# Kernel tuning notes

Hardware: AMD Instinct MI355X
Metric: run time of the kernel (lower is better)

The kernel has to match this reference:

```python
import jax, jax.numpy as jnp
import numpy as np
import math

L = 32            # one_side_length; seq_len = L*L = 1024
EMBED = 768
NDIM = 16
N_SSM = 768
DIRS = 4
K = DIRS * N_SSM  # kernel_dim = 3072
REPEAT = EMBED // N_SSM
SCALE = math.sqrt(1.0 / NDIM)


def _compute_kernel(A_angle, A_radius, B1p, B2p, C1p, C2p):
    # Polar-parameterized complex diagonal A's (4 transition coeffs), sigmoid B, raw C.
    ang = jax.nn.sigmoid(A_angle) * (2.0 * math.pi)
    rad = jax.nn.sigmoid(A_radius)
    A = (rad * jnp.cos(ang) + 1j * (rad * jnp.sin(ang))).astype(jnp.complex64)  # (4,K,NDIM)
    A1, A2, A3, A4 = A[0], A[1], A[2], A[3]
    sB1 = jax.nn.sigmoid(B1p); sB2 = jax.nn.sigmoid(B2p)
    B1 = (sB1[..., 0] + 1j * sB1[..., 1]).astype(jnp.complex64)   # (K,NDIM)
    B2 = (sB2[..., 0] + 1j * sB2[..., 1]).astype(jnp.complex64)
    C1 = (C1p[..., 0] + 1j * C1p[..., 1]).astype(jnp.complex64)
    C2 = (C2p[..., 0] + 1j * C2p[..., 1]).astype(jnp.complex64)

    zeros = jnp.zeros((L, K, NDIM), jnp.complex64)

    # 2-D SSM impulse response (same math the torch module precomputes via the
    # vandermonde / coefficient-table expansion):
    #   x_h[i,j] = A1 x_h[i,j-1] + A2 x_v[i,j-1] + B1 delta[i,j]
    #   x_v[i,j] = A3 x_h[i-1,j] + A4 x_v[i-1,j] + B2 delta[i,j]
    #   k[i,j]   = scale * Re(C1 . x_h[i,j] + C2 . x_v[i,j])
    def row_step(carry, i):
        xh_prev, xv_prev = carry                    # row i-1 states, (L,K,NDIM)
        first = (i == 0).astype(jnp.float32)
        xv = A3 * xh_prev + A4 * xv_prev            # vertical flow from row above
        xv = xv.at[0].add(first * B2)               # impulse at (0,0)
        h0 = (first * B1).astype(jnp.complex64)     # x_h[i,0]
        def col_step(h, v_left):
            h_new = A1 * h + A2 * v_left            # horizontal flow within the row
            return h_new, h_new
        _, xh_rest = jax.lax.scan(col_step, h0, xv[:-1])
        xh = jnp.concatenate([h0[None], xh_rest], axis=0)
        return (xh, xv), (xh, xv)

    (_, _), (XH, XV) = jax.lax.scan(row_step, (zeros, zeros), jnp.arange(L))
    # XH, XV: (L, L, K, NDIM) complex
    k = SCALE * (jnp.einsum('ijhn,hn->ijh', XH, C1) + jnp.einsum('ijhn,hn->ijh', XV, C2))
    # boundary corrections exactly as in the torch module
    k = k.at[0, :, :].multiply(2.0)
    k = k.at[:, 0, :].multiply(2.0)
    k = k.at[0, 0, :].divide(4.0)
    return k.real                                   # (L, L, K) float32


def _forward(x, A_angle, A_radius, B1p, B2p, C1p, C2p, omega):
    S, B, D = x.shape
    residual = x * omega
    k = _compute_kernel(A_angle, A_radius, B1p, B2p, C1p, C2p)
    k = jnp.transpose(k, (2, 0, 1))                 # (K, L, L)
    x4 = jnp.transpose(x, (1, 2, 0)).reshape(B, D, L, L)
    s2 = (2 * L, 2 * L)
    flips = [(), (-2,), (-1,), (-2, -1)]
    out = jnp.zeros((B, D, L, L), jnp.float32)
    for idx, fl in enumerate(flips):                # 4 scan directions via flips
        kk = jnp.tile(k[idx * N_SSM:(idx + 1) * N_SSM], (REPEAT, 1, 1))  # (D,L,L)
        xc = jnp.flip(x4, axis=fl) if fl else x4
        kf = jnp.fft.rfft2(kk, s=s2)
        xf = jnp.fft.rfft2(xc, s=s2)
        cur = jnp.fft.irfft2(xf * kf, s=s2)[..., :L, :L]
        out = out + (jnp.flip(cur, axis=fl) if fl else cur)
    out = jnp.transpose(out.reshape(B, D, S), (2, 0, 1))  # back to (S,B,D)
    return jax.nn.silu(out + residual)


def setup_inputs() -> dict:
    key = jax.random.key(0)
    ks = jax.random.split(key, 9)
    x = jax.random.normal(ks[0], (L * L, 16, EMBED), jnp.float32)
    A_angle = jax.random.uniform(ks[1], (4, K, NDIM), jnp.float32, 0.5, 3.0)
    A_radius = jax.random.uniform(ks[2], (4, K, NDIM), jnp.float32, 0.5, 3.0)
    B1p = 0.2 * jax.random.normal(ks[3], (K, NDIM, 2), jnp.float32)
    B2p = 0.2 * jax.random.normal(ks[4], (K, NDIM, 2), jnp.float32)
    C1p = jax.random.normal(ks[5], (K, NDIM, 2), jnp.float32)
    C2p = jax.random.normal(ks[6], (K, NDIM, 2), jnp.float32)
    omega = jax.random.normal(ks[7], (EMBED,), jnp.float32)
    return {"x": x, "A_angle": A_angle, "A_radius": A_radius, "B1p": B1p,
            "B2p": B2p, "C1p": C1p, "C2p": C2p, "omega": omega}


def reference(x, A_angle, A_radius, B1p, B2p, C1p, C2p, omega):
    return _forward(x, A_angle, A_radius, B1p, B2p, C1p, C2p, omega)
```

## Files before the change

### kernel.cpp

```cpp
#include <hip/hip_runtime.h>
#include <cmath>

#define TWO_PI 6.283185307179586476925f

typedef float f2 __attribute__((ext_vector_type(2)));

__device__ __forceinline__ float sigm(float v) { return 1.0f / (1.0f + __expf(-v)); }
__device__ __forceinline__ f2 mnegi(f2 v) { return (f2){v.y, -v.x}; }
__device__ __forceinline__ f2 mposi(f2 v) { return (f2){-v.y, v.x}; }
__device__ __forceinline__ f2 cmulf(f2 a, f2 b) {
    return (f2){a.x, a.x} * b + (f2){a.y, a.y} * mposi(b);
}
__device__ __forceinline__ f2 cms(f2 A, f2 v) {
    return (f2){A.x, A.x} * v + (f2){A.y, A.y} * (f2){-v.y, v.x};
}

template<int CTRL>
__device__ __forceinline__ float dpp0(float v) {
    return __int_as_float(__builtin_amdgcn_update_dpp(
        0, __float_as_int(v), CTRL, 0xf, 0xf, true));
}
template<int CTRL>
__device__ __forceinline__ f2 dpp2(f2 v) {
    return (f2){dpp0<CTRL>(v.x), dpp0<CTRL>(v.y)};
}
#define DPP_SHR1 0x111
#define DPP_SHR2 0x112
#define DPP_SHR4 0x114
#define DPP_ROR8 0x128

__device__ __forceinline__ float swz_xor16(float v) {
    return __int_as_float(__builtin_amdgcn_ds_swizzle(__float_as_int(v), 0x401F));
}

__device__ __forceinline__ int swz(int r, int c) {
    return (r << 6) | (c ^ ((r ^ (r << 3)) & 63));
}

__device__ __forceinline__ int gfidx(int o, int m, int c) {
    return o + (c << 3) + (m << 9);
}

template<bool INV, bool HALF, bool PRUNE>
__device__ __forceinline__ void dft8(f2* x) {
    const float RS = 0.70710678118654752440f;
    f2 t0, t1, t2, t3, t4, t5, t6, t7;
    if (HALF) {
        t0 = x[0]; t4 = x[0]; t1 = x[1]; t5 = x[1];
        t2 = x[2]; t6 = x[2]; t3 = x[3]; t7 = x[3];
    } else {
        t0 = x[0] + x[4]; t4 = x[0] - x[4];
        t1 = x[1] + x[5]; t5 = x[1] - x[5];
        t2 = x[2] + x[6]; t6 = x[2] - x[6];
        t3 = x[3] + x[7]; t7 = x[3] - x[7];
    }
    f2 t5w, t6w, t7w;
    if (!INV) {
        t5w = RS * (t5 + mnegi(t5));
        t6w = mnegi(t6);
        t7w = RS * (mnegi(t7) - t7);
    } else {
        t5w = RS * (t5 - mnegi(t5));
        t6w = mposi(t6);
        t7w = RS * (mposi(t7) - t7);
    }
    f2 u0 = t0 + t2, u2 = t0 - t2, u1 = t1 + t3, dd = t1 - t3;
    f2 u3 = INV ? mposi(dd) : mnegi(dd);
    x[0] = u0 + u1; x[2] = u2 + u3;
    if (!PRUNE) { x[4] = u0 - u1; x[6] = u2 - u3; }
    f2 v0 = t4 + t6w, v2 = t4 - t6w, v1 = t5w + t7w, ee = t5w - t7w;
    f2 v3 = INV ? mposi(ee) : mnegi(ee);
    x[1] = v0 + v1; x[3] = v2 + v3;
    if (!PRUNE) { x[5] = v0 - v1; x[7] = v2 - v3; }
}

__device__ __forceinline__ void make_tw(int o, f2* tw) {
    float s, co;
    __sincosf(-TWO_PI * (float)o / 64.f, &s, &co);
    tw[0] = (f2){co, s};
#pragma unroll
    for (int k = 1; k < 7; ++k) tw[k] = cmulf(tw[k - 1], tw[0]);
}

template<bool INV, bool COL, bool HALF, bool PRUNE>
__device__ __forceinline__ void fft64(f2* a, f2* r, const f2* tw,
                                      int o, int line) {
    dft8<INV, HALF, false>(r);
#pragma unroll
    for (int k = 1; k < 8; ++k) {
        f2 w = tw[k - 1];
        if (INV) w.y = -w.y;
        r[k] = cmulf(r[k], w);
    }
#pragma unroll
    for (int m = 0; m < 8; ++m) {
        int s = 8 * o + m;
        a[COL ? swz(s, line) : swz(line, s)] = r[m];
    }
#pragma unroll
    for (int j = 0; j < 8; ++j) {
        int s = 8 * j + o;
        r[j] = a[COL ? swz(s, line) : swz(line, s)];
    }
    dft8<INV, false, PRUNE>(r);
}

__global__ __launch_bounds__(512) void ssm_tin(
        const float* __restrict__ Aang, const float* __restrict__ Arad,
        const float* __restrict__ B1p, const float* __restrict__ B2p,
        const float* __restrict__ C1p, const float* __restrict__ C2p,
        f2* __restrict__ Gf, const float* __restrict__ x,
        float* __restrict__ xT) {
    __shared__ __align__(16) char smem[35840];
    int tid = threadIdx.x;

    if (blockIdx.x >= 768) {
        float (*tt)[65] = (float (*)[65])smem;
        int bb = blockIdx.x - 768;
        int bR = bb % 192, bS = bb / 192;
        int r0 = bR * 64, s0 = bS * 64;
        int c = tid & 63, w = tid >> 6;
#pragma unroll
        for (int k = 0; k < 8; ++k) {
            int row = w + 8 * k;
            tt[row][c] = x[(size_t)(s0 + row) * 12288 + r0 + c];
        }
        __syncthreads();
#pragma unroll
        for (int k = 0; k < 8; ++k) {
            int row = w + 8 * k;
            xT[(size_t)(r0 + row) * 1024 + s0 + c] = tt[c][row];
        }
        return;
    }

    f2* a = (f2*)smem;
    float* row0 = (float*)(smem + 32768);
    float* col0 = (float*)(smem + 34816);
    int d = blockIdx.x;
    int w = tid >> 6;
    int t = w & 3;
    int nh = w >> 2;
    int lane = tid & 63;
    int jg = lane & 7;
    int n8 = lane >> 3;
    int n = n8 + 8 * nh;
    int ch = t * 768 + d;
    int gid = ch * 16 + n;

    for (int e = tid; e < 4096; e += 512) a[e] = (f2){0.f, 0.f};
    row0[tid] = 0.f;
    if (tid < 256) col0[tid] = 0.f;

    f2 A[4];
#pragma unroll
    for (int q = 0; q < 4; ++q) {
        float ang = sigm(Aang[q * 49152 + gid]) * TWO_PI;
        float rad = sigm(Arad[q * 49152 + gid]);
        float s, co;
        __sincosf(ang, &s, &co);
        A[q] = (f2){rad * co, rad * s};
    }
    f2 A1 = A[0], A2 = A[1], A3 = A[2], A4 = A[3];
    f2 P2 = cms(A1, A1);
    f2 P3 = cms(A1, P2);
    f2 P4 = cms(P2, P2);
    f2 P8 = cms(P4, P4);
    f2 P16 = cms(P8, P8);
    f2 CZ1 = (jg >= 1) ? P4 : (f2){0.f, 0.f};
    f2 CZ2 = (jg >= 2) ? P8 : (f2){0.f, 0.f};
    f2 CZ4 = (jg >= 4) ? P16 : (f2){0.f, 0.f};

    const float2* B1v = (const float2*)B1p;
    const float2* B2v = (const float2*)B2p;
    const float2* C1v = (const float2*)C1p;
    const float2* C2v = (const float2*)C2p;
    float2 b1 = B1v[gid], b2 = B2v[gid], c1 = C1v[gid], c2 = C2v[gid];
    f2 B1 = (f2){sigm(b1.x), sigm(b1.y)};
    f2 B2 = (f2){sigm(b2.x), sigm(b2.y)};
    float c1r = c1.x, c1i = c1.y, c2r = c2.x, c2i = c2.y;

    f2 pw = (f2){1.f, 0.f};
    if (jg & 1) pw = P4;
    if (jg & 2) pw = cms(pw, P8);
    if (jg & 4) pw = cms(pw, P16);
    f2 EB = cms(pw, B1);

    int bb0 = n8 & 1, bb1 = (n8 >> 1) & 1;
    int col = 4 * jg + 2 * bb0 + bb1;
    int ccl = (t & 2) ? ((64 - col) & 63) : col;

    __syncthreads();

    f2 xv[4], xh[4];
#pragma unroll
    for (int m = 0; m < 4; ++m) { xv[m] = (f2){0.f, 0.f}; xh[m] = (f2){0.f, 0.f}; }

    auto body = [&](int i, bool is0) {
#pragma unroll
        for (int m = 0; m < 4; ++m) xv[m] = cms(A3, xh[m]) + cms(A4, xv[m]);
        if (is0 && jg == 0) xv[0] += B2;
        f2 g1 = cms(A2, xv[0]);
        f2 g2 = cms(A1, g1) + cms(A2, xv[1]);
        f2 g3 = cms(A1, g2) + cms(A2, xv[2]);
        f2 V  = cms(A1, g3) + cms(A2, xv[3]);
        V += cms(CZ1, dpp2<DPP_SHR1>(V));
        V += cms(CZ2, dpp2<DPP_SHR2>(V));
        V += cms(CZ4, dpp2<DPP_SHR4>(V));
        f2 E = dpp2<DPP_SHR1>(V);
        if (jg == 0) E = (f2){0.f, 0.f};
        if (is0) E += EB;
        xh[0] = E;
        xh[1] = cms(A1, E) + g1;
        xh[2] = cms(P2, E) + g2;
        xh[3] = cms(P3, E) + g3;
        float v0 = c1r * xh[0].x - c1i * xh[0].y + c2r * xv[0].x - c2i * xv[0].y;
        float v1 = c1r * xh[1].x - c1i * xh[1].y + c2r * xv[1].x - c2i * xv[1].y;
        float v2 = c1r * xh[2].x - c1i * xh[2].y + c2r * xv[2].x - c2i * xv[2].y;
        float v3 = c1r * xh[3].x - c1i * xh[3].y + c2r * xv[3].x - c2i * xv[3].y;
        float s0 = bb0 ? v0 : v2, s1 = bb0 ? v1 : v3;
        float r0 = dpp0<DPP_ROR8>(s0), r1 = dpp0<DPP_ROR8>(s1);
        float q0 = (bb0 ? v2 : v0) + r0;
        float q1 = (bb0 ? v3 : v1) + r1;
        float s2 = bb1 ? q0 : q1;
        float r2 = swz_xor16(s2);
        float qq = (bb1 ? q1 : q0) + r2;
        qq += __shfl_xor(qq, 32, 64);
        if (n8 < 4) {
            if (is0) {
                row0[(((t << 1) | nh) << 6) | ccl] = qq;
            } else if (col == 0) {
                col0[((((t >> 1) << 1) | nh) << 6) | ((t & 1) ? (64 - i) : i)] = qq;
            } else {
                int rr_ = (t & 1) ? (64 - i) : i;
                ((float*)&a[swz(rr_, ccl)])[nh] = qq;
            }
        }
    };
    body(0, true);
#pragma unroll 1
    for (int i = 1; i < 32; ++i) body(i, false);

    __syncthreads();
    for (int e = tid; e < 4096; e += 512) {
        int r = e >> 6, cm = e & 63;
        int c = cm ^ ((r ^ (r << 3)) & 63);
        f2 cv = a[e];
        float v = cv.x + cv.y;
        if (r == 0) {
            v += row0[c] + row0[64 + c] + row0[128 + c] + row0[192 + c]
               + row0[256 + c] + row0[320 + c] + row0[384 + c] + row0[448 + c];
        } else if (c == 0) {
            v += col0[r] + col0[64 + r] + col0[128 + r] + col0[192 + r];
        }
        float f = 0.25f;
        if (r == 0) f *= 2.f;
        if (c == 0) f *= 2.f;
        if (r == 0 && c == 0) f *= 0.25f;
        a[e] = (f2){f * v, 0.f};
    }
    __syncthreads();
    int o = tid & 7;
    f2 tw[7];
    make_tw(o, tw);
    {
        int row = tid >> 3;
        f2 r[8];
#pragma unroll
        for (int j = 0; j < 8; ++j) r[j] = a[swz(row, 8 * j + o)];
        fft64<false, false, false, false>(a, r, tw, o, row);
#pragma unroll
        for (int m = 0; m < 8; ++m) a[swz(row, o + 8 * m)] = r[m];
    }
    __syncthreads();
    {
        int cc = tid >> 3;
        f2 r[8];
#pragma unroll
        for (int j = 0; j < 8; ++j) r[j] = a[swz(8 * j + o, cc)];
        fft64<false, true, false, false>(a, r, tw, o, cc);
#pragma unroll
        for (int m = 0; m < 8; ++m) Gf[d * 4096 + gfidx(o, m, cc)] = r[m];
    }
}

__global__ __launch_bounds__(512) void conv_fft(
        const float* __restrict__ x, float* __restrict__ xT,
        const f2* __restrict__ Gf, const float* __restrict__ omega,
        float* __restrict__ out, int useT) {
    __shared__ f2 a[8192];
    int bid = (blockIdx.x & 7) * 384 + (blockIdx.x >> 3);
    int d = bid >> 2, b0 = (bid & 3) * 4;
    int tid = threadIdx.x;
    int o = tid & 7, grp = tid >> 3;
    int tl = grp >> 5, row = grp & 31;
    f2 tw[7];
    make_tw(o, tw);
    f2* at = a + (tl << 12);
    int btl = b0 + 2 * tl;
    const size_t base0 = (size_t)(btl * 768 + d) * 1024;
    const size_t base1 = (size_t)((btl + 1) * 768 + d) * 1024;
    {
        f2 r[8];
#pragma unroll
        for (int j = 0; j < 4; ++j) {
            int s2 = row * 32 + 8 * j + o;
            if (useT) r[j] = (f2){xT[base0 + s2], xT[base1 + s2]};
            else      r[j] = (f2){x[s2 * 12288 + btl * 768 + d],
                                  x[s2 * 12288 + (btl + 1) * 768 + d]};
        }
#pragma unroll
        for (int j = 4; j < 8; ++j) r[j] = (f2){0.f, 0.f};
        fft64<false, false, true, false>(at, r, tw, o, row);
#pragma unroll
        for (int m = 0; m < 8; ++m) at[swz(row, o + 8 * m)] = r[m];
    }
    __syncthreads();
#pragma unroll 1
    for (int sw = 0; sw < 2; ++sw) {
        f2* ac = a + (sw << 12);
        int c = grp;
        f2 r[8];
#pragma unroll
        for (int j = 0; j < 4; ++j) r[j] = ac[swz(8 * j + o, c)];
#pragma unroll
        for (int j = 4; j < 8; ++j) r[j] = (f2){0.f, 0.f};
        fft64<false, true, true, false>(ac, r, tw, o, c);
#pragma unroll
        for (int m = 0; m < 8; ++m) {
            r[m] = cmulf(r[m], Gf[d * 4096 + gfidx(o, m, c)]);
        }
        fft64<true, true, false, true>(ac, r, tw, o, c);
#pragma unroll
        for (int m = 0; m < 4; ++m) ac[swz(o + 8 * m, c)] = r[m];
    }
    __syncthreads();
    {
        f2 r[8];
#pragma unroll
        for (int j = 0; j < 8; ++j) r[j] = at[swz(row, 8 * j + o)];
        fft64<true, false, false, true>(at, r, tw, o, row);
        float w = omega[d];
        const float inv = 1.0f / 4096.0f;
#pragma unroll
        for (int m = 0; m < 4; ++m) {
            int cc = o + 8 * m;
            int s2 = row * 32 + cc;
            float xa, xb;
            if (useT) { xa = xT[base0 + s2]; xb = xT[base1 + s2]; }
            else {
                xa = x[s2 * 12288 + btl * 768 + d];
                xb = x[s2 * 12288 + (btl + 1) * 768 + d];
            }
            float ya = r[m].x * inv + xa * w;
            float yb = r[m].y * inv + xb * w;
            float oa = ya / (1.0f + __expf(-ya));
            float ob = yb / (1.0f + __expf(-yb));
            if (useT) {
                xT[base0 + s2] = oa;
                xT[base1 + s2] = ob;
            } else {
                out[s2 * 12288 + btl * 768 + d] = oa;
                out[s2 * 12288 + (btl + 1) * 768 + d] = ob;
            }
        }
    }
}

__global__ __launch_bounds__(256) void transpose_out(const float* __restrict__ xT,
                                                     float* __restrict__ out) {
    __shared__ float t[64][65];
    int bR = blockIdx.x % 192, bS = blockIdx.x / 192;
    int r0 = bR * 64, s0 = bS * 64;
    int c = threadIdx.x & 63, w = threadIdx.x >> 6;
#pragma unroll
    for (int k = 0; k < 16; ++k) {
        int row = w + 4 * k;
        t[row][c] = xT[(size_t)(r0 + row) * 1024 + s0 + c];
    }
    __syncthreads();
#pragma unroll
    for (int k = 0; k < 16; ++k) {
        int row = w + 4 * k;
        out[(size_t)(s0 + row) * 12288 + r0 + c] = t[c][row];
    }
}

extern "C" void kernel_launch(void* const* d_in, const int* in_sizes, int n_in,
                              void* d_out, int out_size, void* d_ws, size_t ws_size,
                              hipStream_t stream) {
    const float* x     = (const float*)d_in[0];
    const float* Aang  = (const float*)d_in[1];
    const float* Arad  = (const float*)d_in[2];
    const float* B1p   = (const float*)d_in[3];
    const float* B2p   = (const float*)d_in[4];
    const float* C1p   = (const float*)d_in[5];
    const float* C2p   = (const float*)d_in[6];
    const float* omega = (const float*)d_in[7];
    float* out = (float*)d_out;
    char* ws = (char*)d_ws;

    f2*    Gf = (f2*)ws;
    float* xT = (float*)(ws + 25165824);
    int useT = (ws_size >= (size_t)75497472) ? 1 : 0;

    int grid1 = useT ? 3840 : 768;
    ssm_tin<<<grid1, 512, 0, stream>>>(Aang, Arad, B1p, B2p, C1p, C2p, Gf, x, xT);
    conv_fft<<<3072, 512, 0, stream>>>(x, xT, Gf, omega, out, useT);
    if (useT) transpose_out<<<3072, 256, 0, stream>>>(xT, out);
}
```

Before: 170.9 us.

## Split conv_fft blocks to one batch pair each and keep inputs in registers

Each conv_fft block now handles a single pair of batches with half the shared memory, and the grid doubles to compensate. The column pass runs once across all 64 thread groups instead of looping twice, while the row passes use only half the threads. The residual input is kept in registers from the first load, so x is not read from global memory a second time. The trade-off is half-idle threads during the row phases and less work per block, in exchange for lower LDS use per block and possibly higher occupancy.

```diff
diff --git a/kernel.cpp b/kernel.cpp
--- a/kernel.cpp
+++ b/kernel.cpp
@@ -288,70 +288,64 @@
         const float* __restrict__ x, float* __restrict__ xT,
         const f2* __restrict__ Gf, const float* __restrict__ omega,
         float* __restrict__ out, int useT) {
-    __shared__ f2 a[8192];
-    int bid = (blockIdx.x & 7) * 384 + (blockIdx.x >> 3);
-    int d = bid >> 2, b0 = (bid & 3) * 4;
+    __shared__ f2 a[4096];
+    int bid = (blockIdx.x & 7) * 768 + (blockIdx.x >> 3);
+    int d = bid >> 3, b = (bid & 7) * 2;
     int tid = threadIdx.x;
     int o = tid & 7, grp = tid >> 3;
-    int tl = grp >> 5, row = grp & 31;
     f2 tw[7];
     make_tw(o, tw);
-    f2* at = a + (tl << 12);
-    int btl = b0 + 2 * tl;
-    const size_t base0 = (size_t)(btl * 768 + d) * 1024;
-    const size_t base1 = (size_t)((btl + 1) * 768 + d) * 1024;
-    {
+    const size_t base0 = (size_t)(b * 768 + d) * 1024;
+    const size_t base1 = (size_t)((b + 1) * 768 + d) * 1024;
+    f2 xsave[4];
+    if (grp < 32) {
+        int row = grp;
         f2 r[8];
 #pragma unroll
         for (int j = 0; j < 4; ++j) {
             int s2 = row * 32 + 8 * j + o;
             if (useT) r[j] = (f2){xT[base0 + s2], xT[base1 + s2]};
-            else      r[j] = (f2){x[s2 * 12288 + btl * 768 + d],
-                                  x[s2 * 12288 + (btl + 1) * 768 + d]};
+            else      r[j] = (f2){x[s2 * 12288 + b * 768 + d],
+                                  x[s2 * 12288 + (b + 1) * 768 + d]};
+            xsave[j] = r[j];
         }
 #pragma unroll
         for (int j = 4; j < 8; ++j) r[j] = (f2){0.f, 0.f};
-        fft64<false, false, true, false>(at, r, tw, o, row);
-#pragma unroll
-        for (int m = 0; m < 8; ++m) at[swz(row, o + 8 * m)] = r[m];
-    }
-    __syncthreads();
-#pragma unroll 1
-    for (int sw = 0; sw < 2; ++sw) {
-        f2* ac = a + (sw << 12);
+        fft64<false, false, true, false>(a, r, tw, o, row);
+#pragma unroll
+        for (int m = 0; m < 8; ++m) a[swz(row, o + 8 * m)] = r[m];
+    }
+    __syncthreads();
+    {
         int c = grp;
         f2 r[8];
 #pragma unroll
-        for (int j = 0; j < 4; ++j) r[j] = ac[swz(8 * j + o, c)];
+        for (int j = 0; j < 4; ++j) r[j] = a[swz(8 * j + o, c)];
 #pragma unroll
         for (int j = 4; j < 8; ++j) r[j] = (f2){0.f, 0.f};
-        fft64<false, true, true, false>(ac, r, tw, o, c);
+        fft64<false, true, true, false>(a, r, tw, o, c);
 #pragma unroll
         for (int m = 0; m < 8; ++m) {
             r[m] = cmulf(r[m], Gf[d * 4096 + gfidx(o, m, c)]);
         }
-        fft64<true, true, false, true>(ac, r, tw, o, c);
-#pragma unroll
-        for (int m = 0; m < 4; ++m) ac[swz(o + 8 * m, c)] = r[m];
-    }
-    __syncthreads();
-    {
+        fft64<true, true, false, true>(a, r, tw, o, c);
+#pragma unroll
+        for (int m = 0; m < 4; ++m) a[swz(o + 8 * m, c)] = r[m];
+    }
+    __syncthreads();
+    if (grp < 32) {
+        int row = grp;
         f2 r[8];
 #pragma unroll
-        for (int j = 0; j < 8; ++j) r[j] = at[swz(row, 8 * j + o)];
-        fft64<true, false, false, true>(at, r, tw, o, row);
+        for (int j = 0; j < 8; ++j) r[j] = a[swz(row, 8 * j + o)];
+        fft64<true, false, false, true>(a, r, tw, o, row);
         float w = omega[d];
         const float inv = 1.0f / 4096.0f;
 #pragma unroll
         for (int m = 0; m < 4; ++m) {
             int cc = o + 8 * m;
             int s2 = row * 32 + cc;
-            float xa, xb;
-            if (useT) { xa = xT[base0 + s2]; xb = xT[base1 + s2]; }
-            else {
-                xa = x[s2 * 12288 + btl * 768 + d];
-                xb = x[s2 * 12288 + (btl + 1) * 768 + d];
-            }
+            float xa = xsave[m].x, xb = xsave[m].y;
             float ya = r[m].x * inv + xa * w;
             float yb = r[m].y * inv + xb * w;
             float oa = ya / (1.0f + __expf(-ya));
@@ -360,8 +354,8 @@
                 xT[base0 + s2] = oa;
                 xT[base1 + s2] = ob;
             } else {
-                out[s2 * 12288 + btl * 768 + d] = oa;
-                out[s2 * 12288 + (btl + 1) * 768 + d] = ob;
+                out[s2 * 12288 + b * 768 + d] = oa;
+                out[s2 * 12288 + (b + 1) * 768 + d] = ob;
             }
         }
     }
@@ -406,6 +400,6 @@
 
     int grid1 = useT ? 3840 : 768;
     ssm_tin<<<grid1, 512, 0, stream>>>(Aang, Arad, B1p, B2p, C1p, C2p, Gf, x, xT);
-    conv_fft<<<3072, 512, 0, stream>>>(x, xT, Gf, omega, out, useT);
+    conv_fft<<<6144, 512, 0, stream>>>(x, xT, Gf, omega, out, useT);
     if (useT) transpose_out<<<3072, 256, 0, stream>>>(xT, out);
 }
```

New measurement: 147.5 us. 1.16x faster.
